# Performance work log

Hardware: AMD Instinct MI355X
Metric: run time of the kernel (lower is better)

The kernel has to match this reference:

```python
import jax, jax.numpy as jnp
import numpy as np

WS = (4, 4, 4)      # window size (d, h, w)
SS = (2, 2, 2)      # shift size
HEADS = 4
EPS = 1e-6          # flax LayerNorm default epsilon


def _rel_pos_index(ws):
    # replicates the source exactly (np.meshgrid default 'xy' indexing)
    coords = np.stack(np.meshgrid(np.arange(ws[0]), np.arange(ws[1]), np.arange(ws[2])))
    cf = coords.reshape(3, -1)
    rc = (cf[:, :, None] - cf[:, None, :]).transpose(1, 2, 0).astype(np.int64)
    rc[:, :, 0] += ws[0] - 1
    rc[:, :, 1] += ws[1] - 1
    rc[:, :, 2] += ws[2] - 1
    rc[:, :, 0] *= (2 * ws[1] - 1) * (2 * ws[2] - 1)
    rc[:, :, 1] *= 2 * ws[2] - 1
    return rc.sum(-1)  # (n, n)


def _compute_mask(dp, hp, wp, ws, ss):
    # standard shifted-window attention mask: (nw, n, n) with 0 / -100
    img = np.zeros((1, dp, hp, wp, 1), np.float32)
    cnt = 0
    sls = lambda w, s: (slice(0, -w), slice(-w, -s), slice(-s, None))
    for d in sls(ws[0], ss[0]):
        for h in sls(ws[1], ss[1]):
            for w in sls(ws[2], ss[2]):
                img[:, d, h, w, :] = cnt
                cnt += 1
    mw = img.reshape(1, dp // ws[0], ws[0], hp // ws[1], ws[1], wp // ws[2], ws[2], 1)
    mw = mw.transpose(0, 1, 3, 5, 2, 4, 6, 7).reshape(-1, ws[0] * ws[1] * ws[2])
    am = mw[:, None, :] - mw[:, :, None]
    return np.where(am != 0, np.float32(-100.0), np.float32(0.0))


def window_partition(x, ws):
    b, d, h, w, c = x.shape
    x = x.reshape(b, d // ws[0], ws[0], h // ws[1], ws[1], w // ws[2], ws[2], c)
    return x.transpose(0, 1, 3, 5, 2, 4, 6, 7).reshape(-1, ws[0] * ws[1] * ws[2], c)


def window_reverse(windows, ws, dims):
    b, d, h, w = dims
    x = windows.reshape(b, d // ws[0], h // ws[1], w // ws[2], ws[0], ws[1], ws[2], -1)
    return x.transpose(0, 1, 4, 2, 5, 3, 6, 7).reshape(b, d, h, w, -1)


def layernorm(x, scale, bias):
    m = x.mean(-1, keepdims=True)
    v = x.var(-1, keepdims=True)
    return (x - m) * jax.lax.rsqrt(v + EPS) * scale + bias


def setup_inputs() -> dict:
    key = jax.random.key(0)
    ks = jax.random.split(key, 8)
    B, D, H, W, C = 2, 32, 64, 64, 128
    HID = 4 * C
    p = 0.02
    return {
        "x": jax.random.normal(ks[0], (B, D, H, W, C), jnp.float32),
        "mask": jnp.asarray(_compute_mask(D, H, W, WS, SS)),
        "norm1_scale": jnp.ones((C,), jnp.float32),
        "norm1_bias": jnp.zeros((C,), jnp.float32),
        "qkv_w": jax.random.normal(ks[1], (C, 3 * C), jnp.float32) * p,
        "rel_bias_table": jax.random.normal(ks[2], ((2 * WS[0] - 1) * (2 * WS[1] - 1) * (2 * WS[2] - 1), HEADS), jnp.float32) * p,
        "proj_w": jax.random.normal(ks[3], (C, C), jnp.float32) * p,
        "proj_b": jnp.zeros((C,), jnp.float32),
        "norm2_scale": jnp.ones((C,), jnp.float32),
        "norm2_bias": jnp.zeros((C,), jnp.float32),
        "mlp_w1": jax.random.normal(ks[4], (C, HID), jnp.float32) * p,
        "mlp_b1": jnp.zeros((HID,), jnp.float32),
        "mlp_w2": jax.random.normal(ks[5], (HID, C), jnp.float32) * p,
        "mlp_b2": jnp.zeros((C,), jnp.float32),
    }


def reference(x, mask, norm1_scale, norm1_bias, qkv_w, rel_bias_table, proj_w, proj_b,
              norm2_scale, norm2_bias, mlp_w1, mlp_b1, mlp_w2, mlp_b2):
    b, d, h, w, c = x.shape
    hd = c // HEADS
    scale = hd ** -0.5
    n = WS[0] * WS[1] * WS[2]

    shortcut = x
    xn = layernorm(x, norm1_scale, norm1_bias)
    # cyclic shift + window partition
    shifted = jnp.roll(xn, shift=(-SS[0], -SS[1], -SS[2]), axis=(1, 2, 3))
    xw = window_partition(shifted, WS)                      # (b*nw, n, c)
    bw = xw.shape[0]

    qkv = (xw @ qkv_w).reshape(bw, n, 3, HEADS, hd).transpose(2, 0, 3, 1, 4)
    q, k, v = qkv[0] * scale, qkv[1], qkv[2]                # (bw, heads, n, hd)
    attn = jnp.einsum('bhqd,bhkd->bhqk', q, k)              # (bw, heads, n, n)

    idx = _rel_pos_index(WS)
    bias = rel_bias_table[idx.reshape(-1)].reshape(n, n, HEADS).transpose(2, 0, 1)
    attn = attn + bias[None]

    nw = mask.shape[0]
    attn = attn.reshape(bw // nw, nw, HEADS, n, n) + mask[None, :, None]
    attn = jax.nn.softmax(attn.reshape(bw, HEADS, n, n), axis=-1)

    out = jnp.einsum('bhqk,bhkd->bhqd', attn, v)
    out = jnp.swapaxes(out, 1, 2).reshape(bw, n, c)
    out = out @ proj_w + proj_b

    attn_out = window_reverse(out, WS, (b, d, h, w))
    attn_out = jnp.roll(attn_out, shift=SS, axis=(1, 2, 3))

    x = shortcut + attn_out
    xn2 = layernorm(x, norm2_scale, norm2_bias)
    m = jax.nn.gelu(xn2 @ mlp_w1 + mlp_b1) @ mlp_w2 + mlp_b2
    return x + m
```

## Files before the change

kernel.cpp:

```cpp
#include <hip/hip_runtime.h>

typedef __bf16 bf16x8 __attribute__((ext_vector_type(8)));
typedef float f32x4 __attribute__((ext_vector_type(4)));
typedef unsigned short u16x4 __attribute__((ext_vector_type(4)));
typedef unsigned short u16x8 __attribute__((ext_vector_type(8)));

#define MFMA16(a,b,c) __builtin_amdgcn_mfma_f32_16x16x32_bf16((a),(b),(c),0,0,0)

__device__ __forceinline__ unsigned short f2bf(float f){
  unsigned u = __builtin_bit_cast(unsigned, f);
  u += 0x7FFFu + ((u>>16)&1u);
  return (unsigned short)(u>>16);
}
__device__ __forceinline__ float bf2f(unsigned short h){
  unsigned u = ((unsigned)h)<<16;
  return __builtin_bit_cast(float, u);
}

__device__ __forceinline__ bf16x8 frag_ld(const unsigned short* base, int stride, int tile, int kp, int lane){
  const int row = (lane & 15) + 16*tile;
  const int col = 4*(lane >> 4) + 32*kp;
  const unsigned short* p = base + row*stride + col;
  u16x4 lo = *reinterpret_cast<const u16x4*>(p);
  u16x4 hi = *reinterpret_cast<const u16x4*>(p + 16);
  u16x8 v;
  v[0]=lo[0]; v[1]=lo[1]; v[2]=lo[2]; v[3]=lo[3];
  v[4]=hi[0]; v[5]=hi[1]; v[6]=hi[2]; v[7]=hi[3];
  return __builtin_bit_cast(bf16x8, v);
}

__device__ __forceinline__ bf16x8 afrag_ld(const unsigned short* wf, int mt, int KP, int kp, int lane){
  const unsigned short* p = wf + (size_t)(((mt*KP + kp)<<6) + lane)*8;
  u16x8 v = *reinterpret_cast<const u16x8*>(p);
  return __builtin_bit_cast(bf16x8, v);
}

__global__ void pack_w_kernel(const float* __restrict__ src, unsigned short* __restrict__ dst,
                              int MT, int KP, int M){
  int tid = blockIdx.x*256 + threadIdx.x;
  if (tid >= MT*KP*64) return;
  int lane = tid & 63;
  int t2 = tid >> 6;
  int kp = t2 % KP;
  int mt = t2 / KP;
  int m = 16*mt + (lane & 15);
  int g = lane >> 4;
  u16x8 v;
#pragma unroll
  for (int j = 0; j < 8; ++j) {
    int k = 4*g + (j&3) + 16*(j>>2) + 32*kp;
    v[j] = f2bf(src[k*M + m]);
  }
  *reinterpret_cast<u16x8*>(&dst[(size_t)tid*8]) = v;
}

__global__ void prep_bias_kernel(const float* __restrict__ table, float* __restrict__ biasT){
  int tid = blockIdx.x*256 + threadIdx.x;
  if (tid >= 4*64*64) return;
  int q = tid & 63, key = (tid>>6)&63, h = tid>>12;
  int da = ((q>>2)&3) - ((key>>2)&3) + 3;
  int ha = (q>>4)     - (key>>4)     + 3;
  int wa = (q&3)      - (key&3)      + 3;
  int idx = (da*7 + ha)*7 + wa;
  biasT[tid] = table[idx*4 + h];
}

__global__ __launch_bounds__(256, 2)
void swin_block_kernel(const float* __restrict__ x,
                       const float* __restrict__ n1s, const float* __restrict__ n1b,
                       const unsigned short* __restrict__ wqkv,
                       const float* __restrict__ biasT,
                       const unsigned short* __restrict__ wproj,
                       const float* __restrict__ projb,
                       const float* __restrict__ n2s, const float* __restrict__ n2b,
                       const unsigned short* __restrict__ w1f, const float* __restrict__ b1,
                       const unsigned short* __restrict__ w2f, const float* __restrict__ b2,
                       float* __restrict__ out)
{
  __shared__ unsigned short ldsA[64*140];
  __shared__ unsigned short ldsB[4*6912];
  __shared__ int rid_s[64];

  const int tid  = threadIdx.x;
  const int lane = tid & 63;
  const int w    = tid >> 6;
  const int g    = lane >> 4;
  const int l15  = lane & 15;

  const int wb = blockIdx.x;
  const int b  = wb >> 11;
  const int r0 = wb & 2047;
  const int bd = r0 >> 8, bh = (r0 >> 4) & 15, bwi = r0 & 15;

  const int t = tid >> 2, qtr = tid & 3;
  const int wd = t >> 4, wh = (t >> 2) & 3, ww = t & 3;
  const int dco = (bd*4 + wd + 2) & 31;
  const int hco = (bh*4 + wh + 2) & 63;
  const int wco = (bwi*4 + ww + 2) & 63;
  const long tokl = ((long)((b*32 + dco)*64 + hco))*64 + wco;
  const float* xrow = x + tokl*128 + qtr*32;

  float xr[32];
  float s = 0.f, sq = 0.f;
#pragma unroll
  for (int i = 0; i < 8; ++i) {
    float4 v = reinterpret_cast<const float4*>(xrow)[i];
    xr[4*i+0]=v.x; xr[4*i+1]=v.y; xr[4*i+2]=v.z; xr[4*i+3]=v.w;
    s  += v.x + v.y + v.z + v.w;
    sq += v.x*v.x + v.y*v.y + v.z*v.z + v.w*v.w;
  }
  s  += __shfl_xor(s, 1);  s  += __shfl_xor(s, 2);
  sq += __shfl_xor(sq, 1); sq += __shfl_xor(sq, 2);
  {
    const float mean = s * 0.0078125f;
    const float var  = sq * 0.0078125f - mean*mean;
    const float rs   = rsqrtf(var + 1e-6f);
#pragma unroll
    for (int i = 0; i < 8; ++i) {
      u16x4 o;
#pragma unroll
      for (int j2 = 0; j2 < 4; ++j2) {
        int c = qtr*32 + 4*i + j2;
        o[j2] = f2bf((xr[4*i+j2]-mean)*rs*n1s[c] + n1b[c]);
      }
      *reinterpret_cast<u16x4*>(&ldsA[t*140 + qtr*32 + 4*i]) = o;
    }
  }
  if (tid < 64) {
    int twd = tid >> 4, twh = (tid >> 2) & 3, tww = tid & 3;
    int rd = (bd == 7)  ? (twd < 2 ? 1 : 2) : 0;
    int rh = (bh == 15) ? (twh < 2 ? 1 : 2) : 0;
    int rw = (bwi == 15)? (tww < 2 ? 1 : 2) : 0;
    rid_s[tid] = rd*9 + rh*3 + rw;
  }
  __syncthreads();

  unsigned short* qldsH  = &ldsB[w*6912];
  unsigned short* kldsH  = qldsH + 2304;
  unsigned short* vTldsH = qldsH + 4608;
  unsigned short* pldsH  = qldsH;

  {
    bf16x8 Bx[4][4];
#pragma unroll
    for (int nt = 0; nt < 4; ++nt)
#pragma unroll
      for (int kp = 0; kp < 4; ++kp)
        Bx[nt][kp] = frag_ld(ldsA, 140, nt, kp, lane);

#pragma unroll
    for (int part = 0; part < 3; ++part) {
#pragma unroll
      for (int mi = 0; mi < 2; ++mi) {
        const int mt = part*8 + 2*w + mi;
        bf16x8 A[4];
#pragma unroll
        for (int kp = 0; kp < 4; ++kp) A[kp] = afrag_ld(wqkv, mt, 4, kp, lane);
#pragma unroll
        for (int nt = 0; nt < 4; ++nt) {
          f32x4 acc = {0.f,0.f,0.f,0.f};
#pragma unroll
          for (int kp = 0; kp < 4; ++kp) acc = MFMA16(A[kp], Bx[nt][kp], acc);
          if (part == 0) {
#pragma unroll
            for (int r2 = 0; r2 < 4; ++r2)
              qldsH[(16*nt + l15)*36 + mi*16 + 4*g + r2] = f2bf(acc[r2]*0.17677669529663687f);
          } else if (part == 1) {
#pragma unroll
            for (int r2 = 0; r2 < 4; ++r2)
              kldsH[(16*nt + l15)*36 + mi*16 + 4*g + r2] = f2bf(acc[r2]);
          } else {
#pragma unroll
            for (int r2 = 0; r2 < 4; ++r2)
              vTldsH[(mi*16 + 4*g + r2)*72 + 16*nt + l15] = f2bf(acc[r2]);
          }
        }
      }
    }
  }
  __syncthreads();

  {
    bf16x8 Ak[4], Bq[4];
#pragma unroll
    for (int mt = 0; mt < 4; ++mt) Ak[mt] = frag_ld(kldsH, 36, mt, 0, lane);
#pragma unroll
    for (int nt = 0; nt < 4; ++nt) Bq[nt] = frag_ld(qldsH, 36, nt, 0, lane);
    f32x4 sacc[4][4];
#pragma unroll
    for (int mt = 0; mt < 4; ++mt)
#pragma unroll
      for (int nt = 0; nt < 4; ++nt) {
        f32x4 z = {0.f,0.f,0.f,0.f};
        sacc[mt][nt] = MFMA16(Ak[mt], Bq[nt], z);
      }
    int ridq[4];
#pragma unroll
    for (int nt = 0; nt < 4; ++nt) ridq[nt] = rid_s[16*nt + l15];
#pragma unroll
    for (int mt = 0; mt < 4; ++mt) {
#pragma unroll
      for (int r2 = 0; r2 < 4; ++r2) {
        const int key = 16*mt + 4*g + r2;
        const int ridk = rid_s[key];
#pragma unroll
        for (int nt = 0; nt < 4; ++nt) {
          const int q = 16*nt + l15;
          float add = biasT[(w*64 + key)*64 + q];
          if (ridk != ridq[nt]) add -= 100.f;
          sacc[mt][nt][r2] += add;
        }
      }
    }
#pragma unroll
    for (int nt = 0; nt < 4; ++nt) {
      float mx = -1e30f;
#pragma unroll
      for (int mt = 0; mt < 4; ++mt)
#pragma unroll
        for (int r2 = 0; r2 < 4; ++r2) mx = fmaxf(mx, sacc[mt][nt][r2]);
      mx = fmaxf(mx, __shfl_xor(mx, 16));
      mx = fmaxf(mx, __shfl_xor(mx, 32));
      float sum = 0.f;
#pragma unroll
      for (int mt = 0; mt < 4; ++mt)
#pragma unroll
        for (int r2 = 0; r2 < 4; ++r2) {
          float p = __expf(sacc[mt][nt][r2] - mx);
          sacc[mt][nt][r2] = p; sum += p;
        }
      sum += __shfl_xor(sum, 16);
      sum += __shfl_xor(sum, 32);
      const float inv = 1.f / sum;
#pragma unroll
      for (int mt = 0; mt < 4; ++mt)
#pragma unroll
        for (int r2 = 0; r2 < 4; ++r2)
          pldsH[(16*nt + l15)*72 + 16*mt + 4*g + r2] = f2bf(sacc[mt][nt][r2]*inv);
    }
    bf16x8 Av[2][2];
#pragma unroll
    for (int mt2 = 0; mt2 < 2; ++mt2)
#pragma unroll
      for (int kp = 0; kp < 2; ++kp) Av[mt2][kp] = frag_ld(vTldsH, 72, mt2, kp, lane);
#pragma unroll
    for (int nt = 0; nt < 4; ++nt) {
      bf16x8 Bp[2];
#pragma unroll
      for (int kp = 0; kp < 2; ++kp) Bp[kp] = frag_ld(pldsH, 72, nt, kp, lane);
#pragma unroll
      for (int mt2 = 0; mt2 < 2; ++mt2) {
        f32x4 acc = {0.f,0.f,0.f,0.f};
        acc = MFMA16(Av[mt2][0], Bp[0], acc);
        acc = MFMA16(Av[mt2][1], Bp[1], acc);
#pragma unroll
        for (int r2 = 0; r2 < 4; ++r2)
          ldsA[(16*nt + l15)*140 + w*32 + mt2*16 + 4*g + r2] = f2bf(acc[r2]);
      }
    }
  }
  __syncthreads();

  {
    bf16x8 Bo[4][4];
#pragma unroll
    for (int nt = 0; nt < 4; ++nt)
#pragma unroll
      for (int kp = 0; kp < 4; ++kp)
        Bo[nt][kp] = frag_ld(ldsA, 140, nt, kp, lane);
    f32x4 pacc[2][4];
#pragma unroll
    for (int mi = 0; mi < 2; ++mi) {
      const int mt = 2*w + mi;
      bf16x8 A[4];
#pragma unroll
      for (int kp = 0; kp < 4; ++kp) A[kp] = afrag_ld(wproj, mt, 4, kp, lane);
#pragma unroll
      for (int nt = 0; nt < 4; ++nt) {
        f32x4 acc = {0.f,0.f,0.f,0.f};
#pragma unroll
        for (int kp = 0; kp < 4; ++kp) acc = MFMA16(A[kp], Bo[nt][kp], acc);
        pacc[mi][nt] = acc;
      }
    }
#pragma unroll
    for (int mi = 0; mi < 2; ++mi)
#pragma unroll
      for (int r2 = 0; r2 < 4; ++r2) {
        const float pb = projb[16*(2*w+mi) + 4*g + r2];
#pragma unroll
        for (int nt = 0; nt < 4; ++nt) pacc[mi][nt][r2] += pb;
      }
    __syncthreads();
#pragma unroll
    for (int mi = 0; mi < 2; ++mi)
#pragma unroll
      for (int nt = 0; nt < 4; ++nt)
#pragma unroll
        for (int r2 = 0; r2 < 4; ++r2)
          ldsA[(16*nt + l15)*140 + 16*(2*w+mi) + 4*g + r2] = f2bf(pacc[mi][nt][r2]);
  }
  __syncthreads();

  {
    float s2 = 0.f, sq2 = 0.f;
#pragma unroll
    for (int i = 0; i < 8; ++i) {
      u16x4 av = *reinterpret_cast<const u16x4*>(&ldsA[t*140 + qtr*32 + 4*i]);
#pragma unroll
      for (int j2 = 0; j2 < 4; ++j2) {
        float v2 = xr[4*i+j2] + bf2f(av[j2]);
        xr[4*i+j2] = v2;
        s2 += v2; sq2 += v2*v2;
      }
    }
    s2  += __shfl_xor(s2, 1);  s2  += __shfl_xor(s2, 2);
    sq2 += __shfl_xor(sq2, 1); sq2 += __shfl_xor(sq2, 2);
    const float mean2 = s2*0.0078125f;
    const float rs2 = rsqrtf(sq2*0.0078125f - mean2*mean2 + 1e-6f);
#pragma unroll
    for (int i = 0; i < 8; ++i) {
      u16x4 o;
#pragma unroll
      for (int j2 = 0; j2 < 4; ++j2) {
        int c = qtr*32 + 4*i + j2;
        o[j2] = f2bf((xr[4*i+j2]-mean2)*rs2*n2s[c] + n2b[c]);
      }
      *reinterpret_cast<u16x4*>(&ldsA[t*140 + qtr*32 + 4*i]) = o;
    }
  }
  __syncthreads();

  {
    unsigned short* hid = ldsB;
    bf16x8 Bn[4][4];
#pragma unroll
    for (int nt = 0; nt < 4; ++nt)
#pragma unroll
      for (int kp = 0; kp < 4; ++kp)
        Bn[nt][kp] = frag_ld(ldsA, 140, nt, kp, lane);

    f32x4 macc[2][4];
#pragma unroll
    for (int mi = 0; mi < 2; ++mi)
#pragma unroll
      for (int nt = 0; nt < 4; ++nt) { f32x4 z = {0.f,0.f,0.f,0.f}; macc[mi][nt] = z; }

#pragma unroll
    for (int cc = 0; cc < 2; ++cc) {
#pragma unroll
      for (int mi = 0; mi < 4; ++mi) {
        const int mtl = 4*w + mi;
        const int mtg = cc*16 + mtl;
        bf16x8 A[4];
#pragma unroll
        for (int kp = 0; kp < 4; ++kp) A[kp] = afrag_ld(w1f, mtg, 4, kp, lane);
#pragma unroll
        for (int nt = 0; nt < 4; ++nt) {
          f32x4 acc = {0.f,0.f,0.f,0.f};
#pragma unroll
          for (int kp = 0; kp < 4; ++kp) acc = MFMA16(A[kp], Bn[nt][kp], acc);
#pragma unroll
          for (int r2 = 0; r2 < 4; ++r2) {
            const int hch = 16*mtg + 4*g + r2;
            float v2 = acc[r2] + b1[hch];
            float gg = 0.7978845608028654f*(v2 + 0.044715f*v2*v2*v2);
            float ge = v2 / (1.f + __expf(-2.f*gg));
            hid[(16*nt + l15)*268 + 16*mtl + 4*g + r2] = f2bf(ge);
          }
        }
      }
      __syncthreads();
#pragma unroll
      for (int mi = 0; mi < 2; ++mi) {
        const int mt = 2*w + mi;
        bf16x8 A2[8];
#pragma unroll
        for (int kp = 0; kp < 8; ++kp) A2[kp] = afrag_ld(w2f, mt, 16, cc*8 + kp, lane);
#pragma unroll
        for (int nt = 0; nt < 4; ++nt) {
          f32x4 acc = macc[mi][nt];
#pragma unroll
          for (int kp = 0; kp < 8; ++kp) {
            bf16x8 Bh = frag_ld(hid, 268, nt, kp, lane);
            acc = MFMA16(A2[kp], Bh, acc);
          }
          macc[mi][nt] = acc;
        }
      }
      __syncthreads();
    }
#pragma unroll
    for (int mi = 0; mi < 2; ++mi)
#pragma unroll
      for (int r2 = 0; r2 < 4; ++r2) {
        const float bb = b2[16*(2*w+mi) + 4*g + r2];
#pragma unroll
        for (int nt = 0; nt < 4; ++nt)
          ldsA[(16*nt + l15)*140 + 16*(2*w+mi) + 4*g + r2] = f2bf(macc[mi][nt][r2] + bb);
      }
  }
  __syncthreads();

  {
    float* orow = out + tokl*128 + qtr*32;
#pragma unroll
    for (int i = 0; i < 8; ++i) {
      u16x4 mv = *reinterpret_cast<const u16x4*>(&ldsA[t*140 + qtr*32 + 4*i]);
      float4 v;
      v.x = xr[4*i+0] + bf2f(mv[0]);
      v.y = xr[4*i+1] + bf2f(mv[1]);
      v.z = xr[4*i+2] + bf2f(mv[2]);
      v.w = xr[4*i+3] + bf2f(mv[3]);
      reinterpret_cast<float4*>(orow)[i] = v;
    }
  }
}

extern "C" void kernel_launch(void* const* d_in, const int* in_sizes, int n_in,
                              void* d_out, int out_size, void* d_ws, size_t ws_size,
                              hipStream_t stream) {
  (void)in_sizes; (void)n_in; (void)out_size; (void)ws_size;
  const float* x    = (const float*)d_in[0];
  const float* n1s  = (const float*)d_in[2];
  const float* n1b  = (const float*)d_in[3];
  const float* qkvw = (const float*)d_in[4];
  const float* tbl  = (const float*)d_in[5];
  const float* pw   = (const float*)d_in[6];
  const float* pb   = (const float*)d_in[7];
  const float* n2s  = (const float*)d_in[8];
  const float* n2b  = (const float*)d_in[9];
  const float* w1   = (const float*)d_in[10];
  const float* b1   = (const float*)d_in[11];
  const float* w2   = (const float*)d_in[12];
  const float* b2   = (const float*)d_in[13];
  float* out = (float*)d_out;

  unsigned short* wqkv_f  = (unsigned short*)d_ws;
  unsigned short* wproj_f = wqkv_f  + 24*4*64*8;
  unsigned short* w1_f    = wproj_f + 8*4*64*8;
  unsigned short* w2_f    = w1_f    + 32*4*64*8;
  float*          biasT   = (float*)(w2_f + 8*16*64*8);

  pack_w_kernel<<<(24*4*64 + 255)/256, 256, 0, stream>>>(qkvw, wqkv_f, 24, 4, 384);
  pack_w_kernel<<<(8*4*64  + 255)/256, 256, 0, stream>>>(pw,   wproj_f, 8, 4, 128);
  pack_w_kernel<<<(32*4*64 + 255)/256, 256, 0, stream>>>(w1,   w1_f,   32, 4, 512);
  pack_w_kernel<<<(8*16*64 + 255)/256, 256, 0, stream>>>(w2,   w2_f,    8,16, 128);
  prep_bias_kernel<<<(4*64*64 + 255)/256, 256, 0, stream>>>(tbl, biasT);

  swin_block_kernel<<<4096, 256, 0, stream>>>(x, n1s, n1b, wqkv_f, biasT, wproj_f, pb,
                                              n2s, n2b, w1_f, b1, w2_f, b2, out);
}
```

Before: 569.5 us.

## Keep Q/K/V and P in registers and use fragment-packed LDS layout

Q, K, V and the softmax probabilities now stay in registers as MFMA fragments instead of round-tripping through per-wave LDS buffers. The shared activation and hidden buffers use a fragment-packed layout, so each operand is one 16-byte LDS read. The relative-position bias is pre-permuted to the accumulator layout so it loads as float4. The MLP hidden dimension is processed in four 128-wide chunks. Total LDS use drops and launch bounds rise to 4 blocks per CU, which adds register pressure and a spill risk. The residual is now held in bf16 instead of fp32, which lowers accuracy.

```diff
diff --git a/kernel.cpp b/kernel.cpp
--- a/kernel.cpp
+++ b/kernel.cpp
@@ -16,24 +16,13 @@
   unsigned u = ((unsigned)h)<<16;
   return __builtin_bit_cast(float, u);
 }
-
-__device__ __forceinline__ bf16x8 frag_ld(const unsigned short* base, int stride, int tile, int kp, int lane){
-  const int row = (lane & 15) + 16*tile;
-  const int col = 4*(lane >> 4) + 32*kp;
-  const unsigned short* p = base + row*stride + col;
-  u16x4 lo = *reinterpret_cast<const u16x4*>(p);
-  u16x4 hi = *reinterpret_cast<const u16x4*>(p + 16);
-  u16x8 v;
-  v[0]=lo[0]; v[1]=lo[1]; v[2]=lo[2]; v[3]=lo[3];
-  v[4]=hi[0]; v[5]=hi[1]; v[6]=hi[2]; v[7]=hi[3];
-  return __builtin_bit_cast(bf16x8, v);
-}
-
-__device__ __forceinline__ bf16x8 afrag_ld(const unsigned short* wf, int mt, int KP, int kp, int lane){
-  const unsigned short* p = wf + (size_t)(((mt*KP + kp)<<6) + lane)*8;
-  u16x8 v = *reinterpret_cast<const u16x8*>(p);
-  return __builtin_bit_cast(bf16x8, v);
-}
+__device__ __forceinline__ bf16x8 g_frag(const unsigned short* __restrict__ wf, int fragIdx, int lane){
+  return __builtin_bit_cast(bf16x8, *reinterpret_cast<const u16x8*>(wf + (size_t)(fragIdx*64 + lane)*8));
+}
+__device__ __forceinline__ bf16x8 lds_frag(const unsigned short* base, int fragIdx, int lane){
+  return __builtin_bit_cast(bf16x8, *reinterpret_cast<const u16x8*>(base + (fragIdx*64 + lane)*8));
+}
+__device__ __forceinline__ bf16x8 bc(u16x8 v){ return __builtin_bit_cast(bf16x8, v); }
 
 __global__ void pack_w_kernel(const float* __restrict__ src, unsigned short* __restrict__ dst,
                               int MT, int KP, int M){
@@ -42,8 +31,7 @@
   int lane = tid & 63;
   int t2 = tid >> 6;
   int kp = t2 % KP;
-  int mt = t2 / KP;
-  int m = 16*mt + (lane & 15);
+  int m = 16*(t2 / KP) + (lane & 15);
   int g = lane >> 4;
   u16x8 v;
 #pragma unroll
@@ -54,22 +42,24 @@
   *reinterpret_cast<u16x8*>(&dst[(size_t)tid*8]) = v;
 }
 
-__global__ void prep_bias_kernel(const float* __restrict__ table, float* __restrict__ biasT){
-  int tid = blockIdx.x*256 + threadIdx.x;
-  if (tid >= 4*64*64) return;
-  int q = tid & 63, key = (tid>>6)&63, h = tid>>12;
+__global__ void prep_bias_kernel(const float* __restrict__ table, float* __restrict__ bias2){
+  int o = blockIdx.x*256 + threadIdx.x;
+  if (o >= 4*4*4*64*4) return;
+  int r2 = o&3, lane = (o>>2)&63, nt = (o>>8)&3, mt = (o>>10)&3, h = o>>12;
+  int g = lane>>4, l15 = lane&15;
+  int key = 16*mt + 4*g + r2, q = 16*nt + l15;
   int da = ((q>>2)&3) - ((key>>2)&3) + 3;
   int ha = (q>>4)     - (key>>4)     + 3;
   int wa = (q&3)      - (key&3)      + 3;
-  int idx = (da*7 + ha)*7 + wa;
-  biasT[tid] = table[idx*4 + h];
-}
-
-__global__ __launch_bounds__(256, 2)
+  bias2[o] = table[((da*7+ha)*7+wa)*4 + h];
+}
+
+__global__ __launch_bounds__(256, 4)
 void swin_block_kernel(const float* __restrict__ x,
                        const float* __restrict__ n1s, const float* __restrict__ n1b,
-                       const unsigned short* __restrict__ wqkv,
-                       const float* __restrict__ biasT,
+                       const unsigned short* __restrict__ wqk,
+                       const unsigned short* __restrict__ wvb,
+                       const float* __restrict__ bias2,
                        const unsigned short* __restrict__ wproj,
                        const float* __restrict__ projb,
                        const float* __restrict__ n2s, const float* __restrict__ n2b,
@@ -77,8 +67,8 @@
                        const unsigned short* __restrict__ w2f, const float* __restrict__ b2,
                        float* __restrict__ out)
 {
-  __shared__ unsigned short ldsA[64*140];
-  __shared__ unsigned short ldsB[4*6912];
+  __shared__ __align__(16) unsigned short ldsA[16*64*8];
+  __shared__ __align__(16) unsigned short ldsH[16*64*8];
   __shared__ int rid_s[64];
 
   const int tid  = threadIdx.x;
@@ -99,31 +89,33 @@
   const int wco = (bwi*4 + ww + 2) & 63;
   const long tokl = ((long)((b*32 + dco)*64 + hco))*64 + wco;
   const float* xrow = x + tokl*128 + qtr*32;
-
-  float xr[32];
-  float s = 0.f, sq = 0.f;
-#pragma unroll
-  for (int i = 0; i < 8; ++i) {
-    float4 v = reinterpret_cast<const float4*>(xrow)[i];
-    xr[4*i+0]=v.x; xr[4*i+1]=v.y; xr[4*i+2]=v.z; xr[4*i+3]=v.w;
-    s  += v.x + v.y + v.z + v.w;
-    sq += v.x*v.x + v.y*v.y + v.z*v.z + v.w*v.w;
-  }
-  s  += __shfl_xor(s, 1);  s  += __shfl_xor(s, 2);
-  sq += __shfl_xor(sq, 1); sq += __shfl_xor(sq, 2);
-  {
+  const int tileT = t >> 4, l15t = t & 15;
+
+  u16x8 rsd[4];
+  {
+    float xr[32];
+    float s = 0.f, sq = 0.f;
+#pragma unroll
+    for (int i = 0; i < 8; ++i) {
+      float4 v = reinterpret_cast<const float4*>(xrow)[i];
+      xr[4*i+0]=v.x; xr[4*i+1]=v.y; xr[4*i+2]=v.z; xr[4*i+3]=v.w;
+      s  += v.x + v.y + v.z + v.w;
+      sq += v.x*v.x + v.y*v.y + v.z*v.z + v.w*v.w;
+    }
+    s  += __shfl_xor(s, 1);  s  += __shfl_xor(s, 2);
+    sq += __shfl_xor(sq, 1); sq += __shfl_xor(sq, 2);
     const float mean = s * 0.0078125f;
-    const float var  = sq * 0.0078125f - mean*mean;
-    const float rs   = rsqrtf(var + 1e-6f);
+    const float rs   = rsqrtf(sq * 0.0078125f - mean*mean + 1e-6f);
 #pragma unroll
     for (int i = 0; i < 8; ++i) {
-      u16x4 o;
+      u16x4 o4;
 #pragma unroll
       for (int j2 = 0; j2 < 4; ++j2) {
         int c = qtr*32 + 4*i + j2;
-        o[j2] = f2bf((xr[4*i+j2]-mean)*rs*n1s[c] + n1b[c]);
-      }
-      *reinterpret_cast<u16x4*>(&ldsA[t*140 + qtr*32 + 4*i]) = o;
+        o4[j2] = f2bf((xr[4*i+j2]-mean)*rs*n1s[c] + n1b[c]);
+        rsd[i>>1][4*(i&1)+j2] = f2bf(xr[4*i+j2]);
+      }
+      *reinterpret_cast<u16x4*>(&ldsA[((tileT*4+qtr)*64 + l15t + 16*(i&3))*8 + 4*(i>>2)]) = o4;
     }
   }
   if (tid < 64) {
@@ -135,182 +127,204 @@
   }
   __syncthreads();
 
-  unsigned short* qldsH  = &ldsB[w*6912];
-  unsigned short* kldsH  = qldsH + 2304;
-  unsigned short* vTldsH = qldsH + 4608;
-  unsigned short* pldsH  = qldsH;
-
-  {
-    bf16x8 Bx[4][4];
-#pragma unroll
-    for (int nt = 0; nt < 4; ++nt)
-#pragma unroll
-      for (int kp = 0; kp < 4; ++kp)
-        Bx[nt][kp] = frag_ld(ldsA, 140, nt, kp, lane);
-
-#pragma unroll
-    for (int part = 0; part < 3; ++part) {
-#pragma unroll
-      for (int mi = 0; mi < 2; ++mi) {
-        const int mt = part*8 + 2*w + mi;
-        bf16x8 A[4];
-#pragma unroll
-        for (int kp = 0; kp < 4; ++kp) A[kp] = afrag_ld(wqkv, mt, 4, kp, lane);
-#pragma unroll
-        for (int nt = 0; nt < 4; ++nt) {
-          f32x4 acc = {0.f,0.f,0.f,0.f};
-#pragma unroll
-          for (int kp = 0; kp < 4; ++kp) acc = MFMA16(A[kp], Bx[nt][kp], acc);
-          if (part == 0) {
-#pragma unroll
-            for (int r2 = 0; r2 < 4; ++r2)
-              qldsH[(16*nt + l15)*36 + mi*16 + 4*g + r2] = f2bf(acc[r2]*0.17677669529663687f);
-          } else if (part == 1) {
-#pragma unroll
-            for (int r2 = 0; r2 < 4; ++r2)
-              kldsH[(16*nt + l15)*36 + mi*16 + 4*g + r2] = f2bf(acc[r2]);
-          } else {
-#pragma unroll
-            for (int r2 = 0; r2 < 4; ++r2)
-              vTldsH[(mi*16 + 4*g + r2)*72 + 16*nt + l15] = f2bf(acc[r2]);
-          }
-        }
-      }
-    }
-  }
-  __syncthreads();
-
-  {
-    bf16x8 Ak[4], Bq[4];
-#pragma unroll
-    for (int mt = 0; mt < 4; ++mt) Ak[mt] = frag_ld(kldsH, 36, mt, 0, lane);
-#pragma unroll
-    for (int nt = 0; nt < 4; ++nt) Bq[nt] = frag_ld(qldsH, 36, nt, 0, lane);
+  u16x8 Qf[4], Kf[4], Vf[2][2];
+  {
+    f32x4 acc[2][4];
+#pragma unroll
+    for (int mi=0;mi<2;++mi)
+#pragma unroll
+      for (int nt=0;nt<4;++nt){ f32x4 z={0.f,0.f,0.f,0.f}; acc[mi][nt]=z; }
+#pragma unroll
+    for (int kp=0;kp<4;++kp){
+      bf16x8 bx[4];
+#pragma unroll
+      for (int nt=0;nt<4;++nt) bx[nt] = lds_frag(ldsA, nt*4+kp, lane);
+#pragma unroll
+      for (int mi=0;mi<2;++mi){
+        bf16x8 a = g_frag(wqk, (2*w+mi)*4+kp, lane);
+#pragma unroll
+        for (int nt=0;nt<4;++nt) acc[mi][nt] = MFMA16(a, bx[nt], acc[mi][nt]);
+      }
+    }
+#pragma unroll
+    for (int nt=0;nt<4;++nt){
+      u16x8 v;
+#pragma unroll
+      for (int j=0;j<8;++j) v[j] = f2bf(acc[j>>2][nt][j&3]*0.17677669529663687f);
+      Qf[nt]=v;
+    }
+#pragma unroll
+    for (int mi=0;mi<2;++mi)
+#pragma unroll
+      for (int nt=0;nt<4;++nt){ f32x4 z={0.f,0.f,0.f,0.f}; acc[mi][nt]=z; }
+#pragma unroll
+    for (int kp=0;kp<4;++kp){
+      bf16x8 bx[4];
+#pragma unroll
+      for (int nt=0;nt<4;++nt) bx[nt] = lds_frag(ldsA, nt*4+kp, lane);
+#pragma unroll
+      for (int mi=0;mi<2;++mi){
+        bf16x8 a = g_frag(wqk, (8+2*w+mi)*4+kp, lane);
+#pragma unroll
+        for (int nt=0;nt<4;++nt) acc[mi][nt] = MFMA16(a, bx[nt], acc[mi][nt]);
+      }
+    }
+#pragma unroll
+    for (int nt=0;nt<4;++nt){
+      u16x8 v;
+#pragma unroll
+      for (int j=0;j<8;++j) v[j] = f2bf(acc[j>>2][nt][j&3]);
+      Kf[nt]=v;
+    }
+    f32x4 vacc[4][2];
+#pragma unroll
+    for (int mt=0;mt<4;++mt)
+#pragma unroll
+      for (int c2=0;c2<2;++c2){ f32x4 z={0.f,0.f,0.f,0.f}; vacc[mt][c2]=z; }
+#pragma unroll
+    for (int kp=0;kp<4;++kp){
+      bf16x8 ax[4];
+#pragma unroll
+      for (int mt=0;mt<4;++mt) ax[mt] = lds_frag(ldsA, mt*4+kp, lane);
+#pragma unroll
+      for (int c2=0;c2<2;++c2){
+        bf16x8 bv = g_frag(wvb, (2*w+c2)*4+kp, lane);
+#pragma unroll
+        for (int mt=0;mt<4;++mt) vacc[mt][c2] = MFMA16(ax[mt], bv, vacc[mt][c2]);
+      }
+    }
+#pragma unroll
+    for (int c2=0;c2<2;++c2)
+#pragma unroll
+      for (int kpk=0;kpk<2;++kpk){
+        u16x8 v;
+#pragma unroll
+        for (int j=0;j<8;++j) v[j] = f2bf(vacc[(j>>2)+2*kpk][c2][j&3]);
+        Vf[c2][kpk]=v;
+      }
+  }
+  __syncthreads();
+
+  {
     f32x4 sacc[4][4];
 #pragma unroll
-    for (int mt = 0; mt < 4; ++mt)
-#pragma unroll
-      for (int nt = 0; nt < 4; ++nt) {
+    for (int mt=0;mt<4;++mt)
+#pragma unroll
+      for (int nt=0;nt<4;++nt){
         f32x4 z = {0.f,0.f,0.f,0.f};
-        sacc[mt][nt] = MFMA16(Ak[mt], Bq[nt], z);
+        sacc[mt][nt] = MFMA16(bc(Kf[mt]), bc(Qf[nt]), z);
       }
     int ridq[4];
 #pragma unroll
-    for (int nt = 0; nt < 4; ++nt) ridq[nt] = rid_s[16*nt + l15];
-#pragma unroll
-    for (int mt = 0; mt < 4; ++mt) {
-#pragma unroll
-      for (int r2 = 0; r2 < 4; ++r2) {
-        const int key = 16*mt + 4*g + r2;
-        const int ridk = rid_s[key];
-#pragma unroll
-        for (int nt = 0; nt < 4; ++nt) {
-          const int q = 16*nt + l15;
-          float add = biasT[(w*64 + key)*64 + q];
-          if (ridk != ridq[nt]) add -= 100.f;
-          sacc[mt][nt][r2] += add;
-        }
-      }
-    }
-#pragma unroll
-    for (int nt = 0; nt < 4; ++nt) {
+    for (int nt=0;nt<4;++nt) ridq[nt] = rid_s[16*nt + l15];
+#pragma unroll
+    for (int mt=0;mt<4;++mt){
+      int4 rk = *reinterpret_cast<const int4*>(&rid_s[16*mt + 4*g]);
+#pragma unroll
+      for (int nt=0;nt<4;++nt){
+        float4 bv = reinterpret_cast<const float4*>(bias2)[((w*4+mt)*4+nt)*64 + lane];
+        sacc[mt][nt][0] += bv.x + (rk.x != ridq[nt] ? -100.f : 0.f);
+        sacc[mt][nt][1] += bv.y + (rk.y != ridq[nt] ? -100.f : 0.f);
+        sacc[mt][nt][2] += bv.z + (rk.z != ridq[nt] ? -100.f : 0.f);
+        sacc[mt][nt][3] += bv.w + (rk.w != ridq[nt] ? -100.f : 0.f);
+      }
+    }
+    float inv[4];
+#pragma unroll
+    for (int nt=0;nt<4;++nt){
       float mx = -1e30f;
 #pragma unroll
-      for (int mt = 0; mt < 4; ++mt)
-#pragma unroll
-        for (int r2 = 0; r2 < 4; ++r2) mx = fmaxf(mx, sacc[mt][nt][r2]);
+      for (int mt=0;mt<4;++mt)
+#pragma unroll
+        for (int r2=0;r2<4;++r2) mx = fmaxf(mx, sacc[mt][nt][r2]);
       mx = fmaxf(mx, __shfl_xor(mx, 16));
       mx = fmaxf(mx, __shfl_xor(mx, 32));
       float sum = 0.f;
 #pragma unroll
-      for (int mt = 0; mt < 4; ++mt)
-#pragma unroll
-        for (int r2 = 0; r2 < 4; ++r2) {
+      for (int mt=0;mt<4;++mt)
+#pragma unroll
+        for (int r2=0;r2<4;++r2){
           float p = __expf(sacc[mt][nt][r2] - mx);
           sacc[mt][nt][r2] = p; sum += p;
         }
       sum += __shfl_xor(sum, 16);
       sum += __shfl_xor(sum, 32);
-      const float inv = 1.f / sum;
-#pragma unroll
-      for (int mt = 0; mt < 4; ++mt)
-#pragma unroll
-        for (int r2 = 0; r2 < 4; ++r2)
-          pldsH[(16*nt + l15)*72 + 16*mt + 4*g + r2] = f2bf(sacc[mt][nt][r2]*inv);
-    }
-    bf16x8 Av[2][2];
-#pragma unroll
-    for (int mt2 = 0; mt2 < 2; ++mt2)
-#pragma unroll
-      for (int kp = 0; kp < 2; ++kp) Av[mt2][kp] = frag_ld(vTldsH, 72, mt2, kp, lane);
-#pragma unroll
-    for (int nt = 0; nt < 4; ++nt) {
-      bf16x8 Bp[2];
-#pragma unroll
-      for (int kp = 0; kp < 2; ++kp) Bp[kp] = frag_ld(pldsH, 72, nt, kp, lane);
-#pragma unroll
-      for (int mt2 = 0; mt2 < 2; ++mt2) {
-        f32x4 acc = {0.f,0.f,0.f,0.f};
-        acc = MFMA16(Av[mt2][0], Bp[0], acc);
-        acc = MFMA16(Av[mt2][1], Bp[1], acc);
-#pragma unroll
-        for (int r2 = 0; r2 < 4; ++r2)
-          ldsA[(16*nt + l15)*140 + w*32 + mt2*16 + 4*g + r2] = f2bf(acc[r2]);
-      }
-    }
-  }
-  __syncthreads();
-
-  {
-    bf16x8 Bo[4][4];
-#pragma unroll
-    for (int nt = 0; nt < 4; ++nt)
-#pragma unroll
-      for (int kp = 0; kp < 4; ++kp)
-        Bo[nt][kp] = frag_ld(ldsA, 140, nt, kp, lane);
+      inv[nt] = 1.f / sum;
+    }
+    u16x8 Pf[4][2];
+#pragma unroll
+    for (int nt=0;nt<4;++nt)
+#pragma unroll
+      for (int kpk=0;kpk<2;++kpk){
+        u16x8 v;
+#pragma unroll
+        for (int j=0;j<8;++j) v[j] = f2bf(sacc[(j>>2)+2*kpk][nt][j&3]*inv[nt]);
+        Pf[nt][kpk]=v;
+      }
+#pragma unroll
+    for (int nt=0;nt<4;++nt){
+      f32x4 oa[2];
+#pragma unroll
+      for (int c2=0;c2<2;++c2){
+        f32x4 z = {0.f,0.f,0.f,0.f};
+        z = MFMA16(bc(Vf[c2][0]), bc(Pf[nt][0]), z);
+        oa[c2] = MFMA16(bc(Vf[c2][1]), bc(Pf[nt][1]), z);
+      }
+      u16x8 v;
+#pragma unroll
+      for (int j=0;j<8;++j) v[j] = f2bf(oa[j>>2][j&3]);
+      *reinterpret_cast<u16x8*>(&ldsA[((nt*4+w)*64+lane)*8]) = v;
+    }
+  }
+  __syncthreads();
+
+  {
     f32x4 pacc[2][4];
 #pragma unroll
-    for (int mi = 0; mi < 2; ++mi) {
-      const int mt = 2*w + mi;
-      bf16x8 A[4];
-#pragma unroll
-      for (int kp = 0; kp < 4; ++kp) A[kp] = afrag_ld(wproj, mt, 4, kp, lane);
-#pragma unroll
-      for (int nt = 0; nt < 4; ++nt) {
-        f32x4 acc = {0.f,0.f,0.f,0.f};
-#pragma unroll
-        for (int kp = 0; kp < 4; ++kp) acc = MFMA16(A[kp], Bo[nt][kp], acc);
-        pacc[mi][nt] = acc;
-      }
-    }
-#pragma unroll
-    for (int mi = 0; mi < 2; ++mi)
-#pragma unroll
-      for (int r2 = 0; r2 < 4; ++r2) {
+    for (int mi=0;mi<2;++mi)
+#pragma unroll
+      for (int nt=0;nt<4;++nt){ f32x4 z={0.f,0.f,0.f,0.f}; pacc[mi][nt]=z; }
+#pragma unroll
+    for (int kp=0;kp<4;++kp){
+      bf16x8 bo[4];
+#pragma unroll
+      for (int nt=0;nt<4;++nt) bo[nt] = lds_frag(ldsA, nt*4+kp, lane);
+#pragma unroll
+      for (int mi=0;mi<2;++mi){
+        bf16x8 a = g_frag(wproj, (2*w+mi)*4+kp, lane);
+#pragma unroll
+        for (int nt=0;nt<4;++nt) pacc[mi][nt] = MFMA16(a, bo[nt], pacc[mi][nt]);
+      }
+    }
+#pragma unroll
+    for (int mi=0;mi<2;++mi)
+#pragma unroll
+      for (int r2=0;r2<4;++r2){
         const float pb = projb[16*(2*w+mi) + 4*g + r2];
 #pragma unroll
-        for (int nt = 0; nt < 4; ++nt) pacc[mi][nt][r2] += pb;
+        for (int nt=0;nt<4;++nt) pacc[mi][nt][r2] += pb;
       }
     __syncthreads();
 #pragma unroll
-    for (int mi = 0; mi < 2; ++mi)
-#pragma unroll
-      for (int nt = 0; nt < 4; ++nt)
-#pragma unroll
-        for (int r2 = 0; r2 < 4; ++r2)
-          ldsA[(16*nt + l15)*140 + 16*(2*w+mi) + 4*g + r2] = f2bf(pacc[mi][nt][r2]);
-  }
-  __syncthreads();
-
-  {
+    for (int nt=0;nt<4;++nt){
+      u16x8 v;
+#pragma unroll
+      for (int j=0;j<8;++j) v[j] = f2bf(pacc[j>>2][nt][j&3]);
+      *reinterpret_cast<u16x8*>(&ldsA[((nt*4+w)*64+lane)*8]) = v;
+    }
+  }
+  __syncthreads();
+
+  {
+    float xv[32];
     float s2 = 0.f, sq2 = 0.f;
 #pragma unroll
     for (int i = 0; i < 8; ++i) {
-      u16x4 av = *reinterpret_cast<const u16x4*>(&ldsA[t*140 + qtr*32 + 4*i]);
+      u16x4 sg = *reinterpret_cast<const u16x4*>(&ldsA[((tileT*4+qtr)*64 + l15t + 16*(i&3))*8 + 4*(i>>2)]);
 #pragma unroll
       for (int j2 = 0; j2 < 4; ++j2) {
-        float v2 = xr[4*i+j2] + bf2f(av[j2]);
-        xr[4*i+j2] = v2;
+        float v2 = bf2f(rsd[i>>1][4*(i&1)+j2]) + bf2f(sg[j2]);
+        xv[4*i+j2] = v2;
         s2 += v2; sq2 += v2*v2;
       }
     }
@@ -320,85 +334,82 @@
     const float rs2 = rsqrtf(sq2*0.0078125f - mean2*mean2 + 1e-6f);
 #pragma unroll
     for (int i = 0; i < 8; ++i) {
-      u16x4 o;
+      u16x4 o4;
 #pragma unroll
       for (int j2 = 0; j2 < 4; ++j2) {
         int c = qtr*32 + 4*i + j2;
-        o[j2] = f2bf((xr[4*i+j2]-mean2)*rs2*n2s[c] + n2b[c]);
-      }
-      *reinterpret_cast<u16x4*>(&ldsA[t*140 + qtr*32 + 4*i]) = o;
-    }
-  }
-  __syncthreads();
-
-  {
-    unsigned short* hid = ldsB;
-    bf16x8 Bn[4][4];
-#pragma unroll
-    for (int nt = 0; nt < 4; ++nt)
-#pragma unroll
-      for (int kp = 0; kp < 4; ++kp)
-        Bn[nt][kp] = frag_ld(ldsA, 140, nt, kp, lane);
-
+        o4[j2] = f2bf((xv[4*i+j2]-mean2)*rs2*n2s[c] + n2b[c]);
+        rsd[i>>1][4*(i&1)+j2] = f2bf(xv[4*i+j2]);
+      }
+      *reinterpret_cast<u16x4*>(&ldsA[((tileT*4+qtr)*64 + l15t + 16*(i&3))*8 + 4*(i>>2)]) = o4;
+    }
+  }
+  __syncthreads();
+
+  {
     f32x4 macc[2][4];
 #pragma unroll
-    for (int mi = 0; mi < 2; ++mi)
-#pragma unroll
-      for (int nt = 0; nt < 4; ++nt) { f32x4 z = {0.f,0.f,0.f,0.f}; macc[mi][nt] = z; }
-
-#pragma unroll
-    for (int cc = 0; cc < 2; ++cc) {
-#pragma unroll
-      for (int mi = 0; mi < 4; ++mi) {
-        const int mtl = 4*w + mi;
-        const int mtg = cc*16 + mtl;
-        bf16x8 A[4];
-#pragma unroll
-        for (int kp = 0; kp < 4; ++kp) A[kp] = afrag_ld(w1f, mtg, 4, kp, lane);
-#pragma unroll
-        for (int nt = 0; nt < 4; ++nt) {
-          f32x4 acc = {0.f,0.f,0.f,0.f};
-#pragma unroll
-          for (int kp = 0; kp < 4; ++kp) acc = MFMA16(A[kp], Bn[nt][kp], acc);
-#pragma unroll
-          for (int r2 = 0; r2 < 4; ++r2) {
-            const int hch = 16*mtg + 4*g + r2;
-            float v2 = acc[r2] + b1[hch];
-            float gg = 0.7978845608028654f*(v2 + 0.044715f*v2*v2*v2);
-            float ge = v2 / (1.f + __expf(-2.f*gg));
-            hid[(16*nt + l15)*268 + 16*mtl + 4*g + r2] = f2bf(ge);
-          }
+    for (int mi=0;mi<2;++mi)
+#pragma unroll
+      for (int nt=0;nt<4;++nt){ f32x4 z={0.f,0.f,0.f,0.f}; macc[mi][nt]=z; }
+#pragma unroll
+    for (int cc=0;cc<4;++cc){
+      f32x4 hacc[2][4];
+#pragma unroll
+      for (int mi=0;mi<2;++mi)
+#pragma unroll
+        for (int nt=0;nt<4;++nt){ f32x4 z={0.f,0.f,0.f,0.f}; hacc[mi][nt]=z; }
+#pragma unroll
+      for (int kp=0;kp<4;++kp){
+        bf16x8 bn[4];
+#pragma unroll
+        for (int nt=0;nt<4;++nt) bn[nt] = lds_frag(ldsA, nt*4+kp, lane);
+#pragma unroll
+        for (int mi=0;mi<2;++mi){
+          bf16x8 a = g_frag(w1f, (cc*8+2*w+mi)*4+kp, lane);
+#pragma unroll
+          for (int nt=0;nt<4;++nt) hacc[mi][nt] = MFMA16(a, bn[nt], hacc[mi][nt]);
         }
       }
+#pragma unroll
+      for (int nt=0;nt<4;++nt){
+        u16x8 hv;
+#pragma unroll
+        for (int j=0;j<8;++j){
+          const int mi = j>>2, r2 = j&3;
+          const int hch = cc*128 + 32*w + 16*mi + 4*g + r2;
+          float v2 = hacc[mi][nt][r2] + b1[hch];
+          float gg = 0.7978845608028654f*(v2 + 0.044715f*v2*v2*v2);
+          float ge = v2 / (1.f + __expf(-2.f*gg));
+          hv[j] = f2bf(ge);
+        }
+        *reinterpret_cast<u16x8*>(&ldsH[((nt*4+w)*64+lane)*8]) = hv;
+      }
       __syncthreads();
 #pragma unroll
-      for (int mi = 0; mi < 2; ++mi) {
-        const int mt = 2*w + mi;
-        bf16x8 A2[8];
-#pragma unroll
-        for (int kp = 0; kp < 8; ++kp) A2[kp] = afrag_ld(w2f, mt, 16, cc*8 + kp, lane);
-#pragma unroll
-        for (int nt = 0; nt < 4; ++nt) {
-          f32x4 acc = macc[mi][nt];
-#pragma unroll
-          for (int kp = 0; kp < 8; ++kp) {
-            bf16x8 Bh = frag_ld(hid, 268, nt, kp, lane);
-            acc = MFMA16(A2[kp], Bh, acc);
-          }
-          macc[mi][nt] = acc;
+      for (int kph=0;kph<4;++kph){
+        bf16x8 bhf[4];
+#pragma unroll
+        for (int nt=0;nt<4;++nt) bhf[nt] = lds_frag(ldsH, nt*4+kph, lane);
+#pragma unroll
+        for (int mi=0;mi<2;++mi){
+          bf16x8 a2 = g_frag(w2f, (2*w+mi)*16 + cc*4 + kph, lane);
+#pragma unroll
+          for (int nt=0;nt<4;++nt) macc[mi][nt] = MFMA16(a2, bhf[nt], macc[mi][nt]);
         }
       }
       __syncthreads();
     }
 #pragma unroll
-    for (int mi = 0; mi < 2; ++mi)
-#pragma unroll
-      for (int r2 = 0; r2 < 4; ++r2) {
-        const float bb = b2[16*(2*w+mi) + 4*g + r2];
-#pragma unroll
-        for (int nt = 0; nt < 4; ++nt)
-          ldsA[(16*nt + l15)*140 + 16*(2*w+mi) + 4*g + r2] = f2bf(macc[mi][nt][r2] + bb);
-      }
+    for (int nt=0;nt<4;++nt){
+      u16x8 v;
+#pragma unroll
+      for (int j=0;j<8;++j){
+        const int mi = j>>2, r2 = j&3;
+        v[j] = f2bf(macc[mi][nt][r2] + b2[16*(2*w+mi) + 4*g + r2]);
+      }
+      *reinterpret_cast<u16x8*>(&ldsA[((nt*4+w)*64+lane)*8]) = v;
+    }
   }
   __syncthreads();
 
@@ -406,12 +417,12 @@
     float* orow = out + tokl*128 + qtr*32;
 #pragma unroll
     for (int i = 0; i < 8; ++i) {
-      u16x4 mv = *reinterpret_cast<const u16x4*>(&ldsA[t*140 + qtr*32 + 4*i]);
+      u16x4 mv = *reinterpret_cast<const u16x4*>(&ldsA[((tileT*4+qtr)*64 + l15t + 16*(i&3))*8 + 4*(i>>2)]);
       float4 v;
-      v.x = xr[4*i+0] + bf2f(mv[0]);
-      v.y = xr[4*i+1] + bf2f(mv[1]);
-      v.z = xr[4*i+2] + bf2f(mv[2]);
-      v.w = xr[4*i+3] + bf2f(mv[3]);
+      v.x = bf2f(rsd[i>>1][4*(i&1)+0]) + bf2f(mv[0]);
+      v.y = bf2f(rsd[i>>1][4*(i&1)+1]) + bf2f(mv[1]);
+      v.z = bf2f(rsd[i>>1][4*(i&1)+2]) + bf2f(mv[2]);
+      v.w = bf2f(rsd[i>>1][4*(i&1)+3]) + bf2f(mv[3]);
       reinterpret_cast<float4*>(orow)[i] = v;
     }
   }
@@ -436,18 +447,20 @@
   const float* b2   = (const float*)d_in[13];
   float* out = (float*)d_out;
 
-  unsigned short* wqkv_f  = (unsigned short*)d_ws;
-  unsigned short* wproj_f = wqkv_f  + 24*4*64*8;
+  unsigned short* wqk_f   = (unsigned short*)d_ws;
+  unsigned short* wvb_f   = wqk_f   + 16*4*64*8;
+  unsigned short* wproj_f = wvb_f   + 8*4*64*8;
   unsigned short* w1_f    = wproj_f + 8*4*64*8;
   unsigned short* w2_f    = w1_f    + 32*4*64*8;
-  float*          biasT   = (float*)(w2_f + 8*16*64*8);
-
-  pack_w_kernel<<<(24*4*64 + 255)/256, 256, 0, stream>>>(qkvw, wqkv_f, 24, 4, 384);
-  pack_w_kernel<<<(8*4*64  + 255)/256, 256, 0, stream>>>(pw,   wproj_f, 8, 4, 128);
-  pack_w_kernel<<<(32*4*64 + 255)/256, 256, 0, stream>>>(w1,   w1_f,   32, 4, 512);
-  pack_w_kernel<<<(8*16*64 + 255)/256, 256, 0, stream>>>(w2,   w2_f,    8,16, 128);
-  prep_bias_kernel<<<(4*64*64 + 255)/256, 256, 0, stream>>>(tbl, biasT);
-
-  swin_block_kernel<<<4096, 256, 0, stream>>>(x, n1s, n1b, wqkv_f, biasT, wproj_f, pb,
+  float*          bias2   = (float*)(w2_f + 8*16*64*8);
+
+  pack_w_kernel<<<16, 256, 0, stream>>>(qkvw,       wqk_f,  16, 4, 384);
+  pack_w_kernel<<< 8, 256, 0, stream>>>(qkvw + 256, wvb_f,   8, 4, 384);
+  pack_w_kernel<<< 8, 256, 0, stream>>>(pw,   wproj_f, 8, 4, 128);
+  pack_w_kernel<<<32, 256, 0, stream>>>(w1,   w1_f,   32, 4, 512);
+  pack_w_kernel<<<32, 256, 0, stream>>>(w2,   w2_f,    8,16, 128);
+  prep_bias_kernel<<<64, 256, 0, stream>>>(tbl, bias2);
+
+  swin_block_kernel<<<4096, 256, 0, stream>>>(x, n1s, n1b, wqk_f, wvb_f, bias2, wproj_f, pb,
                                               n2s, n2b, w1_f, b1, w2_f, b2, out);
 }
```

Result: slower. 640.2 us (+12.4%).
